# Kernel tuning notes

Measured on AMD Instinct MI355X. Metric: run time of the kernel, lower is better.

Reference implementation:

```python
import jax, jax.numpy as jnp
import numpy as np

S, N, IN = 32, 65536, 2
DYN, GEMB, GH, MAT, CH, OUT = 32, 32, 64, 32, 64, 5
CE = DYN + MAT  # cell_embedding_size = 64


def setup_inputs() -> dict:
    key = jax.random.key(0)
    ks = jax.random.split(key, 12)
    r = lambda k, shape: jax.random.normal(k, shape, jnp.float32) * 0.1
    return {
        "input_data": jax.random.normal(ks[0], (S, N, IN), jnp.float32),
        "cell_h0": jnp.zeros((N, CH), jnp.float32),
        "cell_c0": jnp.zeros((N, CH), jnp.float32),
        "graph_h0": jnp.zeros((N, GH), jnp.float32),
        "graph_c0": jnp.zeros((N, GH), jnp.float32),
        "W_dyn": r(ks[1], (DYN, IN)), "b_dyn": jnp.zeros((DYN,), jnp.float32),
        "W_gemb": r(ks[2], (GEMB, IN)), "b_gemb": jnp.zeros((GEMB,), jnp.float32),
        "Wih_g": r(ks[3], (4 * GH, GEMB)), "Whh_g": r(ks[4], (4 * GH, GH)),
        "bih_g": jnp.zeros((4 * GH,), jnp.float32), "bhh_g": jnp.zeros((4 * GH,), jnp.float32),
        "w_graph": r(ks[5], (GH, MAT)),
        "Wih_c": r(ks[6], (4 * CH, CE)), "Whh_c": r(ks[7], (4 * CH, CH)),
        "bih_c": jnp.zeros((4 * CH,), jnp.float32), "bhh_c": jnp.zeros((4 * CH,), jnp.float32),
        "W_out": r(ks[8], (OUT, CH)), "b_out": jnp.zeros((OUT,), jnp.float32),
        "seq_len": S, "num_nodes": N,
    }


def _lstm_cell(x, h, c, Wih, Whh, bih, bhh):
    # torch nn.LSTMCell gate order: i, f, g, o
    gates = x @ Wih.T + bih + h @ Whh.T + bhh
    i, f, g, o = jnp.split(gates, 4, axis=-1)
    c2 = jax.nn.sigmoid(f) * c + jax.nn.sigmoid(i) * jnp.tanh(g)
    h2 = jax.nn.sigmoid(o) * jnp.tanh(c2)
    return h2, c2


def reference(input_data, cell_h0, cell_c0, graph_h0, graph_c0,
              W_dyn, b_dyn, W_gemb, b_gemb,
              Wih_g, Whh_g, bih_g, bhh_g, w_graph,
              Wih_c, Whh_c, bih_c, bhh_c, W_out, b_out,
              seq_len, num_nodes):
    # dropout is identity (eval mode / p=0)
    def step(carry, frame):
        ch, cc, gh, gc = carry
        dyn = jax.nn.relu(frame @ W_dyn.T + b_dyn)                 # [N, DYN]
        gemb = jax.nn.relu(frame @ W_gemb.T + b_gemb)              # [N, GEMB]
        gh, gc = _lstm_cell(gemb, gh, gc, Wih_g, Whh_g, bih_g, bhh_g)
        # leave-one-out node sum == total sum minus self
        loo = gh.sum(axis=0, keepdims=True) - gh                   # [N, GH]
        graph_feat = loo @ w_graph                                 # [N, MAT]
        cell_emb = jnp.concatenate([dyn, graph_feat], axis=1)      # [N, CE]
        ch, cc = _lstm_cell(cell_emb, ch, cc, Wih_c, Whh_c, bih_c, bhh_c)
        out = ch @ W_out.T + b_out                                 # [N, OUT]
        return (ch, cc, gh, gc), out

    (ch, cc, gh, gc), outputs = jax.lax.scan(
        step, (cell_h0, cell_c0, graph_h0, graph_c0), input_data)
    return outputs, (ch, cc), (gh, gc)
```

## Files before the change

kernel.cpp:

```cpp
#include <hip/hip_runtime.h>
#include <hip/hip_bf16.h>


#define Sx    32
#define Nx    65536
#define OUTx  5
#define KG    96
#define KC    160
#define LWG   104
#define LWC   168
#define GRIDA 256
#define TPB   1024
#define GRIDF 512
#define TPBF  512

typedef __attribute__((ext_vector_type(4))) float f32x4;
typedef __attribute__((ext_vector_type(8))) short bf16x8;
typedef unsigned short ushort;
typedef unsigned int uint;

__device__ __forceinline__ float sigm(float x) {
    return __builtin_amdgcn_rcpf(1.f + __expf(-x));
}
__device__ __forceinline__ float tanh_fast(float x) {
    return fmaf(-2.f, __builtin_amdgcn_rcpf(1.f + __expf(2.f * x)), 1.f);
}
__device__ __forceinline__ ushort f2b(float x) {
    uint u = __float_as_uint(x);
    u += 0x7fffu + ((u >> 16) & 1u);
    return (ushort)(u >> 16);
}
__device__ __forceinline__ ushort f2b_n(float x) {
    __hip_bfloat16 b = __float2bfloat16(x);
    return *reinterpret_cast<ushort*>(&b);
}
__device__ __forceinline__ int swz(int row, int col) {
    return col ^ (((row >> 2) & 3) << 4);
}

__global__ __launch_bounds__(256) void k_prep(
    const float* __restrict__ Wih_g, const float* __restrict__ Whh_g,
    const float* __restrict__ bih_g, const float* __restrict__ bhh_g,
    const float* __restrict__ wgr,
    const float* __restrict__ Wih_c, const float* __restrict__ Whh_c,
    const float* __restrict__ bih_c, const float* __restrict__ bhh_c,
    const float* __restrict__ Wout,
    ushort* __restrict__ Wg, ushort* __restrict__ Wc,
    ushort* __restrict__ WoB,
    float* __restrict__ Wfold2,
    float* __restrict__ bsum_g, float* __restrict__ bC0)
{
    const int tid = blockIdx.x * 256 + threadIdx.x;
    const int nt = gridDim.x * 256;
    for (int idx = tid; idx < 256 * KG; idx += nt) {
        int col = idx / KG, k = idx % KG;
        float v = (k < 32) ? Wih_g[col * 32 + k] : Whh_g[col * 64 + (k - 32)];
        Wg[idx] = f2b(v);
    }
    for (int idx = tid; idx < 256 * KC; idx += nt) {
        int col = idx / KC, k = idx % KC;
        float v;
        if (k < 32) v = Wih_c[col * 64 + k];
        else if (k < 96) {
            int d = k - 32; float a = 0.f;
            for (int j = 0; j < 32; ++j)
                a = fmaf(wgr[d * 32 + j], Wih_c[col * 64 + 32 + j], a);
            v = -a;
        } else v = Whh_c[col * 64 + (k - 96)];
        Wc[idx] = f2b(v);
    }
    for (int idx = tid; idx < 16 * 64; idx += nt) {
        int col = idx >> 6, k = idx & 63;
        WoB[idx] = (col < OUTx) ? f2b(Wout[col * 64 + k]) : (ushort)0;
    }
    for (int idx = tid; idx < 64 * 256; idx += nt) {
        int k = idx >> 8, col = idx & 255;
        float a = 0.f;
        for (int j = 0; j < 32; ++j)
            a = fmaf(wgr[k * 32 + j], Wih_c[col * 64 + 32 + j], a);
        Wfold2[idx] = a;
    }
    if (tid < 256) {
        bsum_g[tid] = bih_g[tid] + bhh_g[tid];
        bC0[tid]    = bih_c[tid] + bhh_c[tid];
    }
}

__global__ __launch_bounds__(TPB, 2) void k_graph_all(
    const float* __restrict__ input,
    const float* __restrict__ gh0, const float* __restrict__ gc0,
    const float* __restrict__ Wge, const float* __restrict__ bge,
    const ushort* __restrict__ Wg, const float* __restrict__ bsum_g,
    float* __restrict__ partials,
    ushort* __restrict__ ghb,
    float* __restrict__ ghf, float* __restrict__ gcf)
{
    const int tid = threadIdx.x;
    const int wave = tid >> 6, lane = tid & 63;
    const int c = lane & 15, g4 = lane >> 4;
    const int nb = blockIdx.x * 256 + wave * 16;
    const int na = nb + c;

    __shared__ __align__(16) ushort lWg[256 * LWG];
    __shared__ __align__(16) ushort t_lds[16][16][72];
    __shared__ float wsum[2][16][64];

    {
        const uint* src = (const uint*)Wg;
        uint* dst = (uint*)lWg;
        for (int i = tid; i < 256 * (KG / 2); i += TPB)
            dst[(i / (KG / 2)) * (LWG / 2) + (i % (KG / 2))] = src[i];
    }
    __syncthreads();

    float bsg[4][4];
#pragma unroll
    for (int q = 0; q < 4; ++q)
#pragma unroll
        for (int g = 0; g < 4; ++g)
            bsg[q][g] = bsum_g[64 * g + 16 * q + c];

    float gcr[4][4];
#pragma unroll
    for (int q = 0; q < 4; ++q)
#pragma unroll
        for (int r = 0; r < 4; ++r)
            gcr[q][r] = gc0[(nb + 4 * g4 + r) * 64 + 16 * q + c];
    bf16x8 agh0, agh1;
#pragma unroll
    for (int j = 0; j < 8; ++j) {
        agh0[j] = (short)f2b(gh0[na * 64 + g4 * 8 + j]);
        agh1[j] = (short)f2b(gh0[na * 64 + 32 + g4 * 8 + j]);
    }

#pragma unroll 1
    for (int t = 0; t < Sx; ++t) {
        const float* frame = input + (size_t)t * Nx * 2;
        const float f0 = frame[2 * na], f1 = frame[2 * na + 1];
        const int lastt = (t == Sx - 1);
        bf16x8 a0;
#pragma unroll
        for (int j = 0; j < 8; ++j) {
            const int k = g4 * 8 + j;
            float v = fmaf(f1, Wge[2 * k + 1], fmaf(f0, Wge[2 * k], bge[k]));
            a0[j] = (short)f2b_n(fmaxf(v, 0.f));
        }
        float hsq[4];
#pragma unroll 2
        for (int q = 0; q < 4; ++q) {
            f32x4 acc[4];
#pragma unroll
            for (int g = 0; g < 4; ++g) {
                acc[g] = (f32x4){0.f, 0.f, 0.f, 0.f};
                const ushort* wp = lWg + (16 * (4 * g + q) + c) * LWG + g4 * 8;
                bf16x8 b0 = *(const bf16x8*)(wp);
                bf16x8 b1 = *(const bf16x8*)(wp + 32);
                bf16x8 b2 = *(const bf16x8*)(wp + 64);
                acc[g] = __builtin_amdgcn_mfma_f32_16x16x32_bf16(a0,   b0, acc[g], 0, 0, 0);
                acc[g] = __builtin_amdgcn_mfma_f32_16x16x32_bf16(agh0, b1, acc[g], 0, 0, 0);
                acc[g] = __builtin_amdgcn_mfma_f32_16x16x32_bf16(agh1, b2, acc[g], 0, 0, 0);
            }
            const int d = 16 * q + c;
            float s_r = 0.f;
#pragma unroll
            for (int r = 0; r < 4; ++r) {
                const float ai = acc[0][r] + bsg[q][0], af = acc[1][r] + bsg[q][1],
                            ag = acc[2][r] + bsg[q][2], ao = acc[3][r] + bsg[q][3];
                const float c2 = fmaf(sigm(af), gcr[q][r], sigm(ai) * tanh_fast(ag));
                gcr[q][r] = c2;
                const float h2 = sigm(ao) * tanh_fast(c2);
                const int row = 4 * g4 + r;
                t_lds[wave][row][swz(row, 16 * q + c)] = f2b(h2);
                if (lastt) {
                    const int n = nb + row;
                    ghf[n * 64 + d] = h2;
                    gcf[n * 64 + d] = c2;
                }
                s_r += h2;
            }
            hsq[q] = s_r;
        }
#pragma unroll
        for (int q = 0; q < 4; ++q) {
            float v = hsq[q];
            v += __shfl_xor(v, 16);
            v += __shfl_xor(v, 32);
            hsq[q] = v;
        }
        if (g4 == 0) {
#pragma unroll
            for (int q = 0; q < 4; ++q) wsum[t & 1][wave][16 * q + c] = hsq[q];
        }
        __syncthreads();
        agh0 = *(const bf16x8*)(&t_lds[wave][c][swz(c, g4 * 8)]);
        agh1 = *(const bf16x8*)(&t_lds[wave][c][swz(c, 32 + g4 * 8)]);
        if (ghb) {
            ushort* gp = ghb + ((size_t)t * Nx + na) * 64 + g4 * 8;
            *(bf16x8*)(gp)      = agh0;
            *(bf16x8*)(gp + 32) = agh1;
        }
        if (tid < 64) {
            float a = 0.f;
#pragma unroll
            for (int w8 = 0; w8 < 16; ++w8) a += wsum[t & 1][w8][tid];
            partials[((size_t)t * GRIDA + blockIdx.x) * 64 + tid] = a;
        }
    }
}

__global__ __launch_bounds__(256) void k_bias(
    const float* __restrict__ partials,
    const float* __restrict__ Wfold2, const float* __restrict__ bC0,
    float* __restrict__ bias_all)
{
    const int t = blockIdx.x, tid = threadIdx.x;
    __shared__ float red[4][64];
    __shared__ float S[64];
    const int d = tid & 63, j = tid >> 6;
    float a = 0.f;
    for (int b = j; b < GRIDA; b += 4)
        a += partials[((size_t)t * GRIDA + b) * 64 + d];
    red[j][d] = a;
    __syncthreads();
    if (tid < 64) S[tid] = red[0][tid] + red[1][tid] + red[2][tid] + red[3][tid];
    __syncthreads();
    float bv = bC0[tid];
#pragma unroll
    for (int k = 0; k < 64; ++k) bv = fmaf(S[k], Wfold2[k * 256 + tid], bv);
    bias_all[t * 256 + tid] = bv;
}

__global__ __launch_bounds__(TPB, 2) void k_cell_pt(
    const float* __restrict__ input,
    const ushort* __restrict__ ghb,
    const float* __restrict__ ch0, const float* __restrict__ cc0,
    const float* __restrict__ Wdy, const float* __restrict__ bdy,
    const ushort* __restrict__ Wc, const float* __restrict__ bias_all,
    const ushort* __restrict__ WoB, const float* __restrict__ bo5,
    float* __restrict__ out0,
    float* __restrict__ chf, float* __restrict__ ccf)
{
    const int tid = threadIdx.x;
    const int wave = tid >> 6, lane = tid & 63;
    const int c = lane & 15, g4 = lane >> 4;
    const int nb = blockIdx.x * 256 + wave * 16;
    const int na = nb + c;

    __shared__ __align__(16) ushort lWc[256 * LWC];
    __shared__ __align__(16) ushort t_lds[16][16][72];

    {
        const uint* src2 = (const uint*)Wc;
        uint* dst2 = (uint*)lWc;
        for (int i = tid; i < 256 * (KC / 2); i += TPB)
            dst2[(i / (KC / 2)) * (LWC / 2) + (i % (KC / 2))] = src2[i];
    }
    __syncthreads();

    float ccr[4][4];
#pragma unroll
    for (int q = 0; q < 4; ++q)
#pragma unroll
        for (int r = 0; r < 4; ++r)
            ccr[q][r] = cc0[(nb + 4 * g4 + r) * 64 + 16 * q + c];
    bf16x8 ach0, ach1;
#pragma unroll
    for (int j = 0; j < 8; ++j) {
        ach0[j] = (short)f2b(ch0[na * 64 + g4 * 8 + j]);
        ach1[j] = (short)f2b(ch0[na * 64 + 32 + g4 * 8 + j]);
    }
    bf16x8 woB0 = *(const bf16x8*)(WoB + c * 64 + g4 * 8);
    bf16x8 woB1 = *(const bf16x8*)(WoB + c * 64 + 32 + g4 * 8);
    const float bo_c = (c < OUTx) ? bo5[c] : 0.f;

#pragma unroll 1
    for (int t = 0; t < Sx; ++t) {
        const float* frame = input + (size_t)t * Nx * 2;
        const float f0 = frame[2 * na], f1 = frame[2 * na + 1];
        const int lastt = (t == Sx - 1);

        const ushort* gp = ghb + ((size_t)t * Nx + na) * 64 + g4 * 8;
        bf16x8 agh0 = *(const bf16x8*)(gp);
        bf16x8 agh1 = *(const bf16x8*)(gp + 32);

        bf16x8 a0c;
#pragma unroll
        for (int j = 0; j < 8; ++j) {
            const int k = g4 * 8 + j;
            float v = fmaf(f1, Wdy[2 * k + 1], fmaf(f0, Wdy[2 * k], bdy[k]));
            a0c[j] = (short)f2b_n(fmaxf(v, 0.f));
        }
#pragma unroll 1
        for (int q = 0; q < 4; ++q) {
            f32x4 acc[4];
#pragma unroll
            for (int g = 0; g < 4; ++g) {
                acc[g] = (f32x4){0.f, 0.f, 0.f, 0.f};
                const ushort* wp = lWc + (16 * (4 * g + q) + c) * LWC + g4 * 8;
                bf16x8 b0 = *(const bf16x8*)(wp);
                bf16x8 b1 = *(const bf16x8*)(wp + 32);
                bf16x8 b2 = *(const bf16x8*)(wp + 64);
                bf16x8 b3 = *(const bf16x8*)(wp + 96);
                bf16x8 b4 = *(const bf16x8*)(wp + 128);
                acc[g] = __builtin_amdgcn_mfma_f32_16x16x32_bf16(a0c,  b0, acc[g], 0, 0, 0);
                acc[g] = __builtin_amdgcn_mfma_f32_16x16x32_bf16(agh0, b1, acc[g], 0, 0, 0);
                acc[g] = __builtin_amdgcn_mfma_f32_16x16x32_bf16(agh1, b2, acc[g], 0, 0, 0);
                acc[g] = __builtin_amdgcn_mfma_f32_16x16x32_bf16(ach0, b3, acc[g], 0, 0, 0);
                acc[g] = __builtin_amdgcn_mfma_f32_16x16x32_bf16(ach1, b4, acc[g], 0, 0, 0);
            }
            const int d = 16 * q + c;
            const float bi = bias_all[t * 256 + d],
                        bf = bias_all[t * 256 + 64 + d],
                        bg = bias_all[t * 256 + 128 + d],
                        bov = bias_all[t * 256 + 192 + d];
#pragma unroll
            for (int r = 0; r < 4; ++r) {
                const float ai = acc[0][r] + bi, af = acc[1][r] + bf,
                            ag = acc[2][r] + bg, ao = acc[3][r] + bov;
                const float c2 = fmaf(sigm(af), ccr[q][r], sigm(ai) * tanh_fast(ag));
                ccr[q][r] = c2;
                const float h2 = sigm(ao) * tanh_fast(c2);
                const int row = 4 * g4 + r;
                t_lds[wave][row][swz(row, 16 * q + c)] = f2b(h2);
                if (lastt) {
                    const int n = nb + row;
                    chf[n * 64 + d] = h2;
                    ccf[n * 64 + d] = c2;
                }
            }
        }
        ach0 = *(const bf16x8*)(&t_lds[wave][c][swz(c, g4 * 8)]);
        ach1 = *(const bf16x8*)(&t_lds[wave][c][swz(c, 32 + g4 * 8)]);

        {
            f32x4 oa = (f32x4){0.f, 0.f, 0.f, 0.f};
            oa = __builtin_amdgcn_mfma_f32_16x16x32_bf16(ach0, woB0, oa, 0, 0, 0);
            oa = __builtin_amdgcn_mfma_f32_16x16x32_bf16(ach1, woB1, oa, 0, 0, 0);
            if (c < OUTx) {
                float* outp = out0 + (size_t)t * Nx * OUTx;
#pragma unroll
                for (int r = 0; r < 4; ++r)
                    outp[(nb + 4 * g4 + r) * OUTx + c] = oa[r] + bo_c;
            }
        }
    }
}

__global__ __launch_bounds__(TPBF, 2) void k_cell_rc(
    const float* __restrict__ input,
    const float* __restrict__ gh0, const float* __restrict__ gc0,
    const float* __restrict__ ch0, const float* __restrict__ cc0,
    const float* __restrict__ Wge, const float* __restrict__ bge,
    const ushort* __restrict__ Wg, const float* __restrict__ bsum_g,
    const float* __restrict__ Wdy, const float* __restrict__ bdy,
    const ushort* __restrict__ Wc, const float* __restrict__ bias_all,
    const ushort* __restrict__ WoB, const float* __restrict__ bo5,
    float* __restrict__ out0,
    float* __restrict__ chf, float* __restrict__ ccf)
{
    const int tid = threadIdx.x;
    const int wave = tid >> 6, lane = tid & 63;
    const int c = lane & 15, g4 = lane >> 4;
    const int nb = blockIdx.x * 128 + wave * 16;
    const int na = nb + c;

    __shared__ __align__(16) ushort lWg[256 * LWG];
    __shared__ __align__(16) ushort lWc[256 * LWC];
    __shared__ __align__(16) ushort t_lds[8][16][72];

    {
        const uint* src = (const uint*)Wg;
        uint* dst = (uint*)lWg;
        for (int i = tid; i < 256 * (KG / 2); i += TPBF)
            dst[(i / (KG / 2)) * (LWG / 2) + (i % (KG / 2))] = src[i];
        const uint* src2 = (const uint*)Wc;
        uint* dst2 = (uint*)lWc;
        for (int i = tid; i < 256 * (KC / 2); i += TPBF)
            dst2[(i / (KC / 2)) * (LWC / 2) + (i % (KC / 2))] = src2[i];
    }
    __syncthreads();

    float gcr[4][4], ccr[4][4];
#pragma unroll
    for (int q = 0; q < 4; ++q)
#pragma unroll
        for (int r = 0; r < 4; ++r) {
            const int n = nb + 4 * g4 + r, d = 16 * q + c;
            gcr[q][r] = gc0[n * 64 + d];
            ccr[q][r] = cc0[n * 64 + d];
        }
    bf16x8 agh0, agh1, ach0, ach1;
#pragma unroll
    for (int j = 0; j < 8; ++j) {
        agh0[j] = (short)f2b(gh0[na * 64 + g4 * 8 + j]);
        agh1[j] = (short)f2b(gh0[na * 64 + 32 + g4 * 8 + j]);
        ach0[j] = (short)f2b(ch0[na * 64 + g4 * 8 + j]);
        ach1[j] = (short)f2b(ch0[na * 64 + 32 + g4 * 8 + j]);
    }
    bf16x8 woB0 = *(const bf16x8*)(WoB + c * 64 + g4 * 8);
    bf16x8 woB1 = *(const bf16x8*)(WoB + c * 64 + 32 + g4 * 8);
    const float bo_c = (c < OUTx) ? bo5[c] : 0.f;

#pragma unroll 1
    for (int t = 0; t < Sx; ++t) {
        const float* frame = input + (size_t)t * Nx * 2;
        const float f0 = frame[2 * na], f1 = frame[2 * na + 1];
        const int lastt = (t == Sx - 1);

        bf16x8 a0;
#pragma unroll
        for (int j = 0; j < 8; ++j) {
            const int k = g4 * 8 + j;
            float v = fmaf(f1, Wge[2 * k + 1], fmaf(f0, Wge[2 * k], bge[k]));
            a0[j] = (short)f2b(fmaxf(v, 0.f));
        }
#pragma unroll 1
        for (int q = 0; q < 4; ++q) {
            f32x4 acc[4];
#pragma unroll
            for (int g = 0; g < 4; ++g) {
                acc[g] = (f32x4){0.f, 0.f, 0.f, 0.f};
                const ushort* wp = lWg + (16 * (4 * g + q) + c) * LWG + g4 * 8;
                bf16x8 b0 = *(const bf16x8*)(wp);
                bf16x8 b1 = *(const bf16x8*)(wp + 32);
                bf16x8 b2 = *(const bf16x8*)(wp + 64);
                acc[g] = __builtin_amdgcn_mfma_f32_16x16x32_bf16(a0,   b0, acc[g], 0, 0, 0);
                acc[g] = __builtin_amdgcn_mfma_f32_16x16x32_bf16(agh0, b1, acc[g], 0, 0, 0);
                acc[g] = __builtin_amdgcn_mfma_f32_16x16x32_bf16(agh1, b2, acc[g], 0, 0, 0);
            }
            const int d = 16 * q + c;
            const float bi = bsum_g[d], bf = bsum_g[64 + d],
                        bg = bsum_g[128 + d], bo = bsum_g[192 + d];
#pragma unroll
            for (int r = 0; r < 4; ++r) {
                const float ai = acc[0][r] + bi, af = acc[1][r] + bf,
                            ag = acc[2][r] + bg, ao = acc[3][r] + bo;
                const float c2 = fmaf(sigm(af), gcr[q][r], sigm(ai) * tanh_fast(ag));
                gcr[q][r] = c2;
                const float h2 = sigm(ao) * tanh_fast(c2);
                t_lds[wave][4 * g4 + r][16 * q + c] = f2b(h2);
            }
        }
        agh0 = *(const bf16x8*)(&t_lds[wave][c][g4 * 8]);
        agh1 = *(const bf16x8*)(&t_lds[wave][c][32 + g4 * 8]);

        bf16x8 a0c;
#pragma unroll
        for (int j = 0; j < 8; ++j) {
            const int k = g4 * 8 + j;
            float v = fmaf(f1, Wdy[2 * k + 1], fmaf(f0, Wdy[2 * k], bdy[k]));
            a0c[j] = (short)f2b(fmaxf(v, 0.f));
        }
#pragma unroll 1
        for (int q = 0; q < 4; ++q) {
            f32x4 acc[4];
#pragma unroll
            for (int g = 0; g < 4; ++g) {
                acc[g] = (f32x4){0.f, 0.f, 0.f, 0.f};
                const ushort* wp = lWc + (16 * (4 * g + q) + c) * LWC + g4 * 8;
                bf16x8 b0 = *(const bf16x8*)(wp);
                bf16x8 b1 = *(const bf16x8*)(wp + 32);
                bf16x8 b2 = *(const bf16x8*)(wp + 64);
                bf16x8 b3 = *(const bf16x8*)(wp + 96);
                bf16x8 b4 = *(const bf16x8*)(wp + 128);
                acc[g] = __builtin_amdgcn_mfma_f32_16x16x32_bf16(a0c,  b0, acc[g], 0, 0, 0);
                acc[g] = __builtin_amdgcn_mfma_f32_16x16x32_bf16(agh0, b1, acc[g], 0, 0, 0);
                acc[g] = __builtin_amdgcn_mfma_f32_16x16x32_bf16(agh1, b2, acc[g], 0, 0, 0);
                acc[g] = __builtin_amdgcn_mfma_f32_16x16x32_bf16(ach0, b3, acc[g], 0, 0, 0);
                acc[g] = __builtin_amdgcn_mfma_f32_16x16x32_bf16(ach1, b4, acc[g], 0, 0, 0);
            }
            const int d = 16 * q + c;
            const float bi = bias_all[t * 256 + d],
                        bf = bias_all[t * 256 + 64 + d],
                        bg = bias_all[t * 256 + 128 + d],
                        bov = bias_all[t * 256 + 192 + d];
#pragma unroll
            for (int r = 0; r < 4; ++r) {
                const float ai = acc[0][r] + bi, af = acc[1][r] + bf,
                            ag = acc[2][r] + bg, ao = acc[3][r] + bov;
                const float c2 = fmaf(sigm(af), ccr[q][r], sigm(ai) * tanh_fast(ag));
                ccr[q][r] = c2;
                const float h2 = sigm(ao) * tanh_fast(c2);
                t_lds[wave][4 * g4 + r][16 * q + c] = f2b(h2);
                if (lastt) {
                    const int n = nb + 4 * g4 + r;
                    chf[n * 64 + d] = h2;
                    ccf[n * 64 + d] = c2;
                }
            }
        }
        ach0 = *(const bf16x8*)(&t_lds[wave][c][g4 * 8]);
        ach1 = *(const bf16x8*)(&t_lds[wave][c][32 + g4 * 8]);

        {
            f32x4 oa = (f32x4){0.f, 0.f, 0.f, 0.f};
            oa = __builtin_amdgcn_mfma_f32_16x16x32_bf16(ach0, woB0, oa, 0, 0, 0);
            oa = __builtin_amdgcn_mfma_f32_16x16x32_bf16(ach1, woB1, oa, 0, 0, 0);
            if (c < OUTx) {
                float* outp = out0 + (size_t)t * Nx * OUTx;
#pragma unroll
                for (int r = 0; r < 4; ++r)
                    outp[(nb + 4 * g4 + r) * OUTx + c] = oa[r] + bo_c;
            }
        }
    }
}

extern "C" void kernel_launch(void* const* d_in, const int* in_sizes, int n_in,
                              void* d_out, int out_size, void* d_ws, size_t ws_size,
                              hipStream_t stream) {
    const float* input   = (const float*)d_in[0];
    const float* cell_h0 = (const float*)d_in[1];
    const float* cell_c0 = (const float*)d_in[2];
    const float* graph_h0= (const float*)d_in[3];
    const float* graph_c0= (const float*)d_in[4];
    const float* W_dyn   = (const float*)d_in[5];
    const float* b_dyn   = (const float*)d_in[6];
    const float* W_gemb  = (const float*)d_in[7];
    const float* b_gemb  = (const float*)d_in[8];
    const float* Wih_g   = (const float*)d_in[9];
    const float* Whh_g   = (const float*)d_in[10];
    const float* bih_g   = (const float*)d_in[11];
    const float* bhh_g   = (const float*)d_in[12];
    const float* w_graph = (const float*)d_in[13];
    const float* Wih_c   = (const float*)d_in[14];
    const float* Whh_c   = (const float*)d_in[15];
    const float* bih_c   = (const float*)d_in[16];
    const float* bhh_c   = (const float*)d_in[17];
    const float* W_out   = (const float*)d_in[18];
    const float* b_out   = (const float*)d_in[19];

    float* out0 = (float*)d_out;
    float* chf = out0 + (size_t)Sx * Nx * OUTx;
    float* ccf = chf + (size_t)Nx * 64;
    float* ghf = ccf + (size_t)Nx * 64;
    float* gcf = ghf + (size_t)Nx * 64;

    size_t off = 0;
    char* base = (char*)d_ws;
    float*  partials= (float*)(base + off); off += (size_t)Sx * GRIDA * 64 * 4;
    float*  bias_all= (float*)(base + off); off += (size_t)Sx * 256 * 4;
    ushort* Wg      = (ushort*)(base + off); off += 256 * KG * 2;
    ushort* Wc      = (ushort*)(base + off); off += 256 * KC * 2;
    ushort* WoB     = (ushort*)(base + off); off += 16 * 64 * 2;
    float*  Wfold2  = (float*)(base + off); off += 64 * 256 * 4;
    float*  bsum_g  = (float*)(base + off); off += 256 * 4;
    float*  bC0     = (float*)(base + off); off += 256 * 4;
    off = (off + 255) & ~(size_t)255;
    const size_t ghb_bytes = (size_t)Sx * Nx * 64 * 2;
    const bool use_pt = (ws_size >= off + ghb_bytes);
    ushort* ghb = use_pt ? (ushort*)(base + off) : (ushort*)nullptr;

    k_prep<<<64, 256, 0, stream>>>(Wih_g, Whh_g, bih_g, bhh_g, w_graph,
                                   Wih_c, Whh_c, bih_c, bhh_c, W_out,
                                   Wg, Wc, WoB, Wfold2, bsum_g, bC0);

    k_graph_all<<<GRIDA, TPB, 0, stream>>>(input, graph_h0, graph_c0,
                                           W_gemb, b_gemb, Wg, bsum_g,
                                           partials, ghb, ghf, gcf);

    k_bias<<<Sx, 256, 0, stream>>>(partials, Wfold2, bC0, bias_all);

    if (use_pt) {
        k_cell_pt<<<GRIDA, TPB, 0, stream>>>(input, ghb, cell_h0, cell_c0,
                                             W_dyn, b_dyn, Wc, bias_all,
                                             WoB, b_out, out0, chf, ccf);
    } else {
        k_cell_rc<<<GRIDF, TPBF, 0, stream>>>(input, graph_h0, graph_c0,
                                              cell_h0, cell_c0,
                                              W_gemb, b_gemb, Wg, bsum_g,
                                              W_dyn, b_dyn, Wc, bias_all,
                                              WoB, b_out, out0, chf, ccf);
    }
}
```

Measured before the change: 585.6 us.

## Write per-wave graph partial sums to global to drop per-step block barrier

Adds a templated path in the graph LSTM kernel where each wave writes its own hidden-state column sums straight to a larger global partials buffer. This removes the per-timestep __syncthreads and the LDS reduction by thread 0..63, and the bias kernel now reduces over 4096 wave partials instead of 256 block partials. The workspace is reordered so the ghb buffer comes first and the bigger partials buffer goes at the end, with a fallback when the workspace is too small. It also fully unrolls the graph gate loop, unrolls the cell gate loop by two, and switches the bf16 rounding of h to the f2b_n conversion, at the cost of more global writes, more reduction work in k_bias and more register pressure.

```diff
diff --git a/kernel.cpp b/kernel.cpp
--- a/kernel.cpp
+++ b/kernel.cpp
@@ -11,6 +11,7 @@
 #define LWC   168
 #define GRIDA 256
 #define TPB   1024
+#define NWAVE (GRIDA * 16)
 #define GRIDF 512
 #define TPBF  512
 
@@ -86,6 +87,7 @@
     }
 }
 
+template <int PW>
 __global__ __launch_bounds__(TPB, 2) void k_graph_all(
     const float* __restrict__ input,
     const float* __restrict__ gh0, const float* __restrict__ gc0,
@@ -103,7 +105,7 @@
 
     __shared__ __align__(16) ushort lWg[256 * LWG];
     __shared__ __align__(16) ushort t_lds[16][16][72];
-    __shared__ float wsum[2][16][64];
+    __shared__ float wsum[PW ? 1 : 2][16][64];
 
     {
         const uint* src = (const uint*)Wg;
@@ -146,7 +148,7 @@
             a0[j] = (short)f2b_n(fmaxf(v, 0.f));
         }
         float hsq[4];
-#pragma unroll 2
+#pragma unroll
         for (int q = 0; q < 4; ++q) {
             f32x4 acc[4];
 #pragma unroll
@@ -170,7 +172,7 @@
                 gcr[q][r] = c2;
                 const float h2 = sigm(ao) * tanh_fast(c2);
                 const int row = 4 * g4 + r;
-                t_lds[wave][row][swz(row, 16 * q + c)] = f2b(h2);
+                t_lds[wave][row][swz(row, 16 * q + c)] = f2b_n(h2);
                 if (lastt) {
                     const int n = nb + row;
                     ghf[n * 64 + d] = h2;
@@ -187,11 +189,18 @@
             v += __shfl_xor(v, 32);
             hsq[q] = v;
         }
-        if (g4 == 0) {
-#pragma unroll
-            for (int q = 0; q < 4; ++q) wsum[t & 1][wave][16 * q + c] = hsq[q];
-        }
-        __syncthreads();
+        if (PW) {
+            float v = (g4 == 0) ? hsq[0] : (g4 == 1) ? hsq[1]
+                    : (g4 == 2) ? hsq[2] : hsq[3];
+            const int gw = blockIdx.x * 16 + wave;
+            partials[((size_t)t * NWAVE + gw) * 64 + 16 * g4 + c] = v;
+        } else {
+            if (g4 == 0) {
+#pragma unroll
+                for (int q = 0; q < 4; ++q) wsum[t & 1][wave][16 * q + c] = hsq[q];
+            }
+            __syncthreads();
+        }
         agh0 = *(const bf16x8*)(&t_lds[wave][c][swz(c, g4 * 8)]);
         agh1 = *(const bf16x8*)(&t_lds[wave][c][swz(c, 32 + g4 * 8)]);
         if (ghb) {
@@ -199,17 +208,20 @@
             *(bf16x8*)(gp)      = agh0;
             *(bf16x8*)(gp + 32) = agh1;
         }
-        if (tid < 64) {
-            float a = 0.f;
-#pragma unroll
-            for (int w8 = 0; w8 < 16; ++w8) a += wsum[t & 1][w8][tid];
-            partials[((size_t)t * GRIDA + blockIdx.x) * 64 + tid] = a;
+        if (!PW) {
+            if (tid < 64) {
+                float a = 0.f;
+#pragma unroll
+                for (int w8 = 0; w8 < 16; ++w8) a += wsum[t & 1][w8][tid];
+                partials[((size_t)t * GRIDA + blockIdx.x) * 64 + tid] = a;
+            }
         }
     }
 }
 
 __global__ __launch_bounds__(256) void k_bias(
     const float* __restrict__ partials,
+    int nw,
     const float* __restrict__ Wfold2, const float* __restrict__ bC0,
     float* __restrict__ bias_all)
 {
@@ -218,8 +230,8 @@
     __shared__ float S[64];
     const int d = tid & 63, j = tid >> 6;
     float a = 0.f;
-    for (int b = j; b < GRIDA; b += 4)
-        a += partials[((size_t)t * GRIDA + b) * 64 + d];
+    for (int b = j; b < nw; b += 4)
+        a += partials[((size_t)t * nw + b) * 64 + d];
     red[j][d] = a;
     __syncthreads();
     if (tid < 64) S[tid] = red[0][tid] + red[1][tid] + red[2][tid] + red[3][tid];
@@ -290,7 +302,7 @@
             float v = fmaf(f1, Wdy[2 * k + 1], fmaf(f0, Wdy[2 * k], bdy[k]));
             a0c[j] = (short)f2b_n(fmaxf(v, 0.f));
         }
-#pragma unroll 1
+#pragma unroll 2
         for (int q = 0; q < 4; ++q) {
             f32x4 acc[4];
 #pragma unroll
@@ -321,7 +333,7 @@
                 ccr[q][r] = c2;
                 const float h2 = sigm(ao) * tanh_fast(c2);
                 const int row = 4 * g4 + r;
-                t_lds[wave][row][swz(row, 16 * q + c)] = f2b(h2);
+                t_lds[wave][row][swz(row, 16 * q + c)] = f2b_n(h2);
                 if (lastt) {
                     const int n = nb + row;
                     chf[n * 64 + d] = h2;
@@ -536,9 +548,20 @@
     float* ghf = ccf + (size_t)Nx * 64;
     float* gcf = ghf + (size_t)Nx * 64;
 
+    const size_t ghb_bytes   = (size_t)Sx * Nx * 64 * 2;
+    const size_t small_bytes = (size_t)Sx * 256 * 4 + 256 * KG * 2 +
+                               256 * KC * 2 + 16 * 64 * 2 +
+                               64 * 256 * 4 + 256 * 4 + 256 * 4 + 1024;
+    const size_t pb_small = (size_t)Sx * GRIDA * 64 * 4;
+    const size_t pb_big   = (size_t)Sx * NWAVE * 64 * 4;
+
+    char* base = (char*)d_ws;
+    const bool use_pt = (ws_size >= ghb_bytes + small_bytes + pb_small);
+    const bool use_pw = use_pt && (ws_size >= ghb_bytes + small_bytes + pb_big);
+
     size_t off = 0;
-    char* base = (char*)d_ws;
-    float*  partials= (float*)(base + off); off += (size_t)Sx * GRIDA * 64 * 4;
+    ushort* ghb = nullptr;
+    if (use_pt) { ghb = (ushort*)base; off += ghb_bytes; }
     float*  bias_all= (float*)(base + off); off += (size_t)Sx * 256 * 4;
     ushort* Wg      = (ushort*)(base + off); off += 256 * KG * 2;
     ushort* Wc      = (ushort*)(base + off); off += 256 * KC * 2;
@@ -547,19 +570,23 @@
     float*  bsum_g  = (float*)(base + off); off += 256 * 4;
     float*  bC0     = (float*)(base + off); off += 256 * 4;
     off = (off + 255) & ~(size_t)255;
-    const size_t ghb_bytes = (size_t)Sx * Nx * 64 * 2;
-    const bool use_pt = (ws_size >= off + ghb_bytes);
-    ushort* ghb = use_pt ? (ushort*)(base + off) : (ushort*)nullptr;
+    float*  partials= (float*)(base + off);
 
     k_prep<<<64, 256, 0, stream>>>(Wih_g, Whh_g, bih_g, bhh_g, w_graph,
                                    Wih_c, Whh_c, bih_c, bhh_c, W_out,
                                    Wg, Wc, WoB, Wfold2, bsum_g, bC0);
 
-    k_graph_all<<<GRIDA, TPB, 0, stream>>>(input, graph_h0, graph_c0,
-                                           W_gemb, b_gemb, Wg, bsum_g,
-                                           partials, ghb, ghf, gcf);
-
-    k_bias<<<Sx, 256, 0, stream>>>(partials, Wfold2, bC0, bias_all);
+    if (use_pw) {
+        k_graph_all<1><<<GRIDA, TPB, 0, stream>>>(input, graph_h0, graph_c0,
+                                                  W_gemb, b_gemb, Wg, bsum_g,
+                                                  partials, ghb, ghf, gcf);
+        k_bias<<<Sx, 256, 0, stream>>>(partials, NWAVE, Wfold2, bC0, bias_all);
+    } else {
+        k_graph_all<0><<<GRIDA, TPB, 0, stream>>>(input, graph_h0, graph_c0,
+                                                  W_gemb, b_gemb, Wg, bsum_g,
+                                                  partials, ghb, ghf, gcf);
+        k_bias<<<Sx, 256, 0, stream>>>(partials, GRIDA, Wfold2, bC0, bias_all);
+    }
 
     if (use_pt) {
         k_cell_pt<<<GRIDA, TPB, 0, stream>>>(input, ghb, cell_h0, cell_c0,
```

After: 1.877 ms. +220.5%, slower.
